# Performance work log

Hardware: AMD Instinct MI355X
Metric: run time of the kernel (lower is better)

Reference implementation:

```python
import jax, jax.numpy as jnp
import numpy as np

EPS = 1e-8

def _conv(x, w, b=None):
    # NCHW conv, stride 1, SAME padding (k=3, pad=1)
    y = jax.lax.conv_general_dilated(x, w, (1, 1), 'SAME',
                                     dimension_numbers=('NCHW', 'OIHW', 'NCHW'))
    if b is not None:
        y = y + b[None, :, None, None]
    return y

def setup_inputs() -> dict:
    key = jax.random.key(0)
    ks = jax.random.split(key, 6)
    B, C, H, W = 512, 1024, 8, 8
    return {
        'x': jax.random.normal(ks[0], (B, C, H, W), jnp.float32),
        'w1_1': jax.random.normal(ks[1], (1, 1, 3, 3), jnp.float32) * 0.1,
        'w5': jax.random.normal(ks[2], (4, 2, 3, 3), jnp.float32) * 0.1,
        'b5': jax.random.normal(ks[3], (4,), jnp.float32) * 0.1,
        'w6': jax.random.normal(ks[4], (1, 4, 3, 3), jnp.float32) * 0.1,
        'b6': jax.random.normal(ks[5], (1,), jnp.float32) * 0.1,
    }

def reference(x, w1_1, w5, b5, w6, b6):
    B, C, H, W = x.shape  # H == W == 8 by module construction
    m = jnp.max(x, axis=1, keepdims=True)  # [B,1,H,W] channel max
    # 2x2 non-overlapping windows, torch unfold layout -> [B,1,(H/2)*(W/2),4]
    win = m.reshape(B, 1, H // 2, 2, W // 2, 2)
    win = win.transpose(0, 1, 2, 4, 3, 5).reshape(B, 1, (H // 2) * (W // 2), 4)
    # probabilistic pooling: clean inf/nan/negatives, sample per window
    winc = jnp.where(jnp.isinf(win) | jnp.isnan(win) | (win < 0), EPS, win)
    skey = jax.random.key(1)
    idx = jax.random.categorical(skey, winc, axis=-1)  # softmax(winc) multinomial
    mo2 = jnp.take_along_axis(winc, idx[..., None], axis=-1)[..., 0]
    mo2 = mo2.reshape(B, 1, H // 2, W // 2)
    # adaptive max/avg pool (4,4) on 8x8 == 2x2 pooling, reuse windows
    mo3 = win.max(axis=-1).reshape(B, 1, H // 2, W // 2)
    ao4 = win.mean(axis=-1).reshape(B, 1, H // 2, W // 2)
    out2 = 0.1 * mo2 + 0.6 * mo3 + 0.3 * ao4
    out2 = _conv(out2, w1_1)  # bias-free 1->1 conv
    out2 = jax.image.resize(out2, (B, 1, H, W), method='bilinear')  # align_corners=False
    out1 = jnp.concatenate([m, out2], axis=1)  # [B,2,H,W]
    gate = jax.nn.sigmoid(_conv(jax.nn.relu(_conv(out1, w5, b5)), w6, b6))  # [B,1,H,W]
    return jax.nn.relu(x * gate)
```

## Files before the change

kernel.cpp:

```cpp
#include <hip/hip_runtime.h>
#include <math.h>

#define C_DIM 1024
#define HW 64
#define NT_A 512
#define NT_B 256
#define F4_PER_BATCH 16384
#define EPSV 1e-8f
#define TINYF 1.17549435e-38f

__device__ __forceinline__ void threefry2x32_01(unsigned x0, unsigned x1,
                                                unsigned& o0, unsigned& o1) {
    const unsigned ks0 = 0u, ks1 = 1u, ks2 = 0x1BD11BDBu;
    x0 += ks0; x1 += ks1;
#define TF_R(r) { x0 += x1; x1 = (x1 << (r)) | (x1 >> (32 - (r))); x1 ^= x0; }
    TF_R(13) TF_R(15) TF_R(26) TF_R(6)
    x0 += ks1; x1 += ks2 + 1u;
    TF_R(17) TF_R(29) TF_R(16) TF_R(24)
    x0 += ks2; x1 += ks0 + 2u;
    TF_R(13) TF_R(15) TF_R(26) TF_R(6)
    x0 += ks0; x1 += ks1 + 3u;
    TF_R(17) TF_R(29) TF_R(16) TF_R(24)
    x0 += ks1; x1 += ks2 + 4u;
    TF_R(13) TF_R(15) TF_R(26) TF_R(6)
    x0 += ks2; x1 += ks0 + 5u;
#undef TF_R
    o0 = x0; o1 = x1;
}

__device__ __forceinline__ unsigned jax_random_bits(unsigned n) {
    unsigned o0, o1;
    threefry2x32_01(0u, n, o0, o1);
    return o0 ^ o1;
}

__device__ __forceinline__ bool bad_val(float v) {
    return ((__float_as_uint(v) & 0x7F800000u) == 0x7F800000u) || (v < 0.0f);
}

__global__ __launch_bounds__(NT_A) void sa_gate_kernel(
    const float* __restrict__ x,
    const float* __restrict__ w11,
    const float* __restrict__ w5,
    const float* __restrict__ b5,
    const float* __restrict__ w6,
    const float* __restrict__ b6,
    float* __restrict__ gate_out)
{
    const int b = blockIdx.x;
    const int t = threadIdx.x;

    const float4* __restrict__ xb = (const float4*)x + (size_t)b * F4_PER_BATCH;

    __shared__ float4 red[8 * 16];
    __shared__ float sm[64];
    __shared__ float sa16[16];
    __shared__ float sb16[16];
    __shared__ float so2[64];
    __shared__ float shid[4 * 64];

    float4 pm = make_float4(-INFINITY, -INFINITY, -INFINITY, -INFINITY);
#pragma unroll 16
    for (int i = 0; i < 32; ++i) {
        float4 v = xb[t + NT_A * i];
        pm.x = fmaxf(pm.x, v.x); pm.y = fmaxf(pm.y, v.y);
        pm.z = fmaxf(pm.z, v.z); pm.w = fmaxf(pm.w, v.w);
    }
#pragma unroll
    for (int off = 16; off <= 32; off <<= 1) {
        pm.x = fmaxf(pm.x, __shfl_xor(pm.x, off, 64));
        pm.y = fmaxf(pm.y, __shfl_xor(pm.y, off, 64));
        pm.z = fmaxf(pm.z, __shfl_xor(pm.z, off, 64));
        pm.w = fmaxf(pm.w, __shfl_xor(pm.w, off, 64));
    }
    const int wv = t >> 6, lane = t & 63;
    if (lane < 16) red[wv * 16 + lane] = pm;
    __syncthreads();
    if (t >= 64) return;

    if (t < 16) {
        float4 a = red[t];
#pragma unroll
        for (int w = 1; w < 8; ++w) {
            float4 o = red[w * 16 + t];
            a.x = fmaxf(a.x, o.x); a.y = fmaxf(a.y, o.y);
            a.z = fmaxf(a.z, o.z); a.w = fmaxf(a.w, o.w);
        }
        sm[t * 4 + 0] = a.x; sm[t * 4 + 1] = a.y;
        sm[t * 4 + 2] = a.z; sm[t * 4 + 3] = a.w;
    }
    __builtin_amdgcn_wave_barrier();

    if (t < 16) {
        int h2 = t >> 2, w2 = t & 3;
        float win[4], winc[4], sg[4];
#pragma unroll
        for (int j = 0; j < 4; ++j) {
            int hh = 2 * h2 + (j >> 1), ww = 2 * w2 + (j & 1);
            float v = sm[hh * 8 + ww];
            win[j] = v;
            winc[j] = bad_val(v) ? EPSV : v;
            unsigned n = (unsigned)(b * 64 + t * 4 + j);
            unsigned bits = jax_random_bits(n);
            float f = __uint_as_float(0x3F800000u | (bits >> 9)) - 1.0f;
            float u = fmaxf(TINYF, f + TINYF);
            sg[j] = -logf(-logf(u));
        }
        int idx = 0;
        float best = winc[0] + sg[0];
#pragma unroll
        for (int j = 1; j < 4; ++j) {
            float s = winc[j] + sg[j];
            if (s > best) { best = s; idx = j; }
        }
        float mo2 = winc[idx];
        float mo3 = fmaxf(fmaxf(win[0], win[1]), fmaxf(win[2], win[3]));
        float ssum = ((win[0] + win[1]) + win[2]) + win[3];
        float ao4 = ssum * 0.25f;
        sa16[t] = 0.1f * mo2 + 0.6f * mo3 + 0.3f * ao4;
    }
    __builtin_amdgcn_wave_barrier();

    if (t < 16) {
        int i = t >> 2, j = t & 3;
        float acc = 0.0f;
#pragma unroll
        for (int dy = -1; dy <= 1; ++dy) {
            int yy = i + dy;
            if (yy < 0 || yy > 3) continue;
#pragma unroll
            for (int dx = -1; dx <= 1; ++dx) {
                int xx = j + dx;
                if (xx < 0 || xx > 3) continue;
                acc += sa16[yy * 4 + xx] * w11[(dy + 1) * 3 + (dx + 1)];
            }
        }
        sb16[t] = acc;
    }
    __builtin_amdgcn_wave_barrier();

    {
        int y = t >> 3, xx2 = t & 7;
        float sy = (y + 0.5f) * 0.5f - 0.5f;
        float sx = (xx2 + 0.5f) * 0.5f - 0.5f;
        float fy = fminf(fmaxf(sy, 0.0f), 3.0f);
        float fx = fminf(fmaxf(sx, 0.0f), 3.0f);
        int iy0 = (int)floorf(fy); int iy1 = min(iy0 + 1, 3); float ry = fy - (float)iy0;
        int ix0 = (int)floorf(fx); int ix1 = min(ix0 + 1, 3); float rx = fx - (float)ix0;
        float v00 = sb16[iy0 * 4 + ix0], v01 = sb16[iy0 * 4 + ix1];
        float v10 = sb16[iy1 * 4 + ix0], v11 = sb16[iy1 * 4 + ix1];
        float top = v00 * (1.0f - rx) + v01 * rx;
        float bot = v10 * (1.0f - rx) + v11 * rx;
        so2[t] = top * (1.0f - ry) + bot * ry;
    }
    __builtin_amdgcn_wave_barrier();

    {
        int y = t >> 3, x2 = t & 7;
        float a0 = b5[0], a1 = b5[1], a2 = b5[2], a3 = b5[3];
#pragma unroll
        for (int dy = -1; dy <= 1; ++dy) {
            int yy = y + dy;
            if (yy < 0 || yy > 7) continue;
#pragma unroll
            for (int dx = -1; dx <= 1; ++dx) {
                int xx = x2 + dx;
                if (xx < 0 || xx > 7) continue;
                float i0 = sm[yy * 8 + xx];
                float i1 = so2[yy * 8 + xx];
                int kk = (dy + 1) * 3 + (dx + 1);
                a0 += i0 * w5[0 * 18 + kk] + i1 * w5[0 * 18 + 9 + kk];
                a1 += i0 * w5[1 * 18 + kk] + i1 * w5[1 * 18 + 9 + kk];
                a2 += i0 * w5[2 * 18 + kk] + i1 * w5[2 * 18 + 9 + kk];
                a3 += i0 * w5[3 * 18 + kk] + i1 * w5[3 * 18 + 9 + kk];
            }
        }
        shid[0 * 64 + t] = fmaxf(a0, 0.0f);
        shid[1 * 64 + t] = fmaxf(a1, 0.0f);
        shid[2 * 64 + t] = fmaxf(a2, 0.0f);
        shid[3 * 64 + t] = fmaxf(a3, 0.0f);
    }
    __builtin_amdgcn_wave_barrier();

    {
        int y = t >> 3, x2 = t & 7;
        float acc = b6[0];
#pragma unroll
        for (int dy = -1; dy <= 1; ++dy) {
            int yy = y + dy;
            if (yy < 0 || yy > 7) continue;
#pragma unroll
            for (int dx = -1; dx <= 1; ++dx) {
                int xx = x2 + dx;
                if (xx < 0 || xx > 7) continue;
                int kk = (dy + 1) * 3 + (dx + 1);
                int p = yy * 8 + xx;
                acc += shid[0 * 64 + p] * w6[0 + kk]
                     + shid[1 * 64 + p] * w6[9 + kk]
                     + shid[2 * 64 + p] * w6[18 + kk]
                     + shid[3 * 64 + p] * w6[27 + kk];
            }
        }
        gate_out[b * 64 + t] = 1.0f / (1.0f + expf(-acc));
    }
}

__global__ __launch_bounds__(NT_B) void sa_apply_kernel(
    const float* __restrict__ x,
    const float* __restrict__ gate,
    float* __restrict__ out)
{
    const int bid = blockIdx.x;
    const int t = threadIdx.x;
    const int b = bid >> 2;
    const size_t base = (size_t)bid * 4096;

    const float4* __restrict__ x4 = (const float4*)x;
    float4* __restrict__ o4 = (float4*)out;

    const float4 gv = ((const float4*)(gate + b * 64))[t & 15];

#pragma unroll 8
    for (int i = 0; i < 16; ++i) {
        size_t idx = base + t + NT_B * i;
        float4 v = x4[idx];
        float4 o;
        o.x = fmaxf(v.x * gv.x, 0.0f);
        o.y = fmaxf(v.y * gv.y, 0.0f);
        o.z = fmaxf(v.z * gv.z, 0.0f);
        o.w = fmaxf(v.w * gv.w, 0.0f);
        o4[idx] = o;
    }
}

extern "C" void kernel_launch(void* const* d_in, const int* in_sizes, int n_in,
                              void* d_out, int out_size, void* d_ws, size_t ws_size,
                              hipStream_t stream) {
    const float* x   = (const float*)d_in[0];
    const float* w11 = (const float*)d_in[1];
    const float* w5  = (const float*)d_in[2];
    const float* b5  = (const float*)d_in[3];
    const float* w6  = (const float*)d_in[4];
    const float* b6  = (const float*)d_in[5];
    float* out  = (float*)d_out;
    float* gate = (float*)d_ws;

    int B = in_sizes[0] / (C_DIM * HW);
    sa_gate_kernel<<<dim3(B), dim3(NT_A), 0, stream>>>(x, w11, w5, b5, w6, b6, gate);
    sa_apply_kernel<<<dim3(B * 4), dim3(NT_B), 0, stream>>>(x, gate, out);
}
```

Baseline: 259.8 us.

## Split channel-max across blocks with atomics, separate tiny middle kernel, nontemporal stores

The channel-max reduction now runs over 4 blocks per batch instead of one 512-thread block. Partial maxima are combined with atomicMax on an order-preserving unsigned encoding of the floats, which gives more parallelism for the memory-bound read of x. The gate computation moves into its own 64-thread kernel. The apply kernel now uses twice as many blocks, each doing half the work, and writes with nontemporal stores. The trade-off is an extra memset and an extra kernel launch, plus atomic traffic.

Measured after the change: 266.4 us. +2.6%, slower.

```diff
diff --git a/kernel.cpp b/kernel.cpp
--- a/kernel.cpp
+++ b/kernel.cpp
@@ -3,11 +3,11 @@
 
 #define C_DIM 1024
 #define HW 64
-#define NT_A 512
-#define NT_B 256
 #define F4_PER_BATCH 16384
 #define EPSV 1e-8f
 #define TINYF 1.17549435e-38f
+
+typedef float vfloat4 __attribute__((ext_vector_type(4)));
 
 __device__ __forceinline__ void threefry2x32_01(unsigned x0, unsigned x1,
                                                 unsigned& o0, unsigned& o1) {
@@ -38,8 +38,59 @@
     return ((__float_as_uint(v) & 0x7F800000u) == 0x7F800000u) || (v < 0.0f);
 }
 
-__global__ __launch_bounds__(NT_A) void sa_gate_kernel(
-    const float* __restrict__ x,
+__device__ __forceinline__ unsigned enc_f32(float f) {
+    unsigned b = __float_as_uint(f);
+    return (b & 0x80000000u) ? ~b : (b | 0x80000000u);
+}
+__device__ __forceinline__ float dec_f32(unsigned u) {
+    unsigned b = (u & 0x80000000u) ? (u ^ 0x80000000u) : ~u;
+    return __uint_as_float(b);
+}
+
+__global__ __launch_bounds__(256) void sa_max_kernel(
+    const float* __restrict__ x, unsigned* __restrict__ maxenc)
+{
+    const int bid = blockIdx.x;
+    const int t = threadIdx.x;
+    const int b = bid >> 2;
+    const float4* __restrict__ xb = (const float4*)x + (size_t)bid * 4096;
+
+    float4 pm = make_float4(-INFINITY, -INFINITY, -INFINITY, -INFINITY);
+#pragma unroll 8
+    for (int i = 0; i < 16; ++i) {
+        float4 v = xb[t + 256 * i];
+        pm.x = fmaxf(pm.x, v.x); pm.y = fmaxf(pm.y, v.y);
+        pm.z = fmaxf(pm.z, v.z); pm.w = fmaxf(pm.w, v.w);
+    }
+#pragma unroll
+    for (int off = 16; off <= 32; off <<= 1) {
+        pm.x = fmaxf(pm.x, __shfl_xor(pm.x, off, 64));
+        pm.y = fmaxf(pm.y, __shfl_xor(pm.y, off, 64));
+        pm.z = fmaxf(pm.z, __shfl_xor(pm.z, off, 64));
+        pm.w = fmaxf(pm.w, __shfl_xor(pm.w, off, 64));
+    }
+    __shared__ float4 red[4][16];
+    const int wv = t >> 6, lane = t & 63;
+    if (lane < 16) red[wv][lane] = pm;
+    __syncthreads();
+    if (t < 16) {
+        float4 a = red[0][t];
+#pragma unroll
+        for (int w = 1; w < 4; ++w) {
+            float4 o = red[w][t];
+            a.x = fmaxf(a.x, o.x); a.y = fmaxf(a.y, o.y);
+            a.z = fmaxf(a.z, o.z); a.w = fmaxf(a.w, o.w);
+        }
+        unsigned* dst = maxenc + b * 64 + t * 4;
+        atomicMax(dst + 0, enc_f32(a.x));
+        atomicMax(dst + 1, enc_f32(a.y));
+        atomicMax(dst + 2, enc_f32(a.z));
+        atomicMax(dst + 3, enc_f32(a.w));
+    }
+}
+
+__global__ __launch_bounds__(64) void sa_middle_kernel(
+    const unsigned* __restrict__ maxenc,
     const float* __restrict__ w11,
     const float* __restrict__ w5,
     const float* __restrict__ b5,
@@ -50,46 +101,14 @@
     const int b = blockIdx.x;
     const int t = threadIdx.x;
 
-    const float4* __restrict__ xb = (const float4*)x + (size_t)b * F4_PER_BATCH;
-
-    __shared__ float4 red[8 * 16];
     __shared__ float sm[64];
     __shared__ float sa16[16];
     __shared__ float sb16[16];
     __shared__ float so2[64];
     __shared__ float shid[4 * 64];
 
-    float4 pm = make_float4(-INFINITY, -INFINITY, -INFINITY, -INFINITY);
-#pragma unroll 16
-    for (int i = 0; i < 32; ++i) {
-        float4 v = xb[t + NT_A * i];
-        pm.x = fmaxf(pm.x, v.x); pm.y = fmaxf(pm.y, v.y);
-        pm.z = fmaxf(pm.z, v.z); pm.w = fmaxf(pm.w, v.w);
-    }
-#pragma unroll
-    for (int off = 16; off <= 32; off <<= 1) {
-        pm.x = fmaxf(pm.x, __shfl_xor(pm.x, off, 64));
-        pm.y = fmaxf(pm.y, __shfl_xor(pm.y, off, 64));
-        pm.z = fmaxf(pm.z, __shfl_xor(pm.z, off, 64));
-        pm.w = fmaxf(pm.w, __shfl_xor(pm.w, off, 64));
-    }
-    const int wv = t >> 6, lane = t & 63;
-    if (lane < 16) red[wv * 16 + lane] = pm;
-    __syncthreads();
-    if (t >= 64) return;
-
-    if (t < 16) {
-        float4 a = red[t];
-#pragma unroll
-        for (int w = 1; w < 8; ++w) {
-            float4 o = red[w * 16 + t];
-            a.x = fmaxf(a.x, o.x); a.y = fmaxf(a.y, o.y);
-            a.z = fmaxf(a.z, o.z); a.w = fmaxf(a.w, o.w);
-        }
-        sm[t * 4 + 0] = a.x; sm[t * 4 + 1] = a.y;
-        sm[t * 4 + 2] = a.z; sm[t * 4 + 3] = a.w;
-    }
-    __builtin_amdgcn_wave_barrier();
+    sm[t] = dec_f32(maxenc[b * 64 + t]);
+    __syncthreads();
 
     if (t < 16) {
         int h2 = t >> 2, w2 = t & 3;
@@ -119,7 +138,7 @@
         float ao4 = ssum * 0.25f;
         sa16[t] = 0.1f * mo2 + 0.6f * mo3 + 0.3f * ao4;
     }
-    __builtin_amdgcn_wave_barrier();
+    __syncthreads();
 
     if (t < 16) {
         int i = t >> 2, j = t & 3;
@@ -137,7 +156,7 @@
         }
         sb16[t] = acc;
     }
-    __builtin_amdgcn_wave_barrier();
+    __syncthreads();
 
     {
         int y = t >> 3, xx2 = t & 7;
@@ -153,7 +172,7 @@
         float bot = v10 * (1.0f - rx) + v11 * rx;
         so2[t] = top * (1.0f - ry) + bot * ry;
     }
-    __builtin_amdgcn_wave_barrier();
+    __syncthreads();
 
     {
         int y = t >> 3, x2 = t & 7;
@@ -180,7 +199,7 @@
         shid[2 * 64 + t] = fmaxf(a2, 0.0f);
         shid[3 * 64 + t] = fmaxf(a3, 0.0f);
     }
-    __builtin_amdgcn_wave_barrier();
+    __syncthreads();
 
     {
         int y = t >> 3, x2 = t & 7;
@@ -205,31 +224,31 @@
     }
 }
 
-__global__ __launch_bounds__(NT_B) void sa_apply_kernel(
+__global__ __launch_bounds__(256) void sa_apply_kernel(
     const float* __restrict__ x,
     const float* __restrict__ gate,
     float* __restrict__ out)
 {
     const int bid = blockIdx.x;
     const int t = threadIdx.x;
-    const int b = bid >> 2;
-    const size_t base = (size_t)bid * 4096;
-
-    const float4* __restrict__ x4 = (const float4*)x;
-    float4* __restrict__ o4 = (float4*)out;
+    const int b = bid >> 3;
+    const size_t base = (size_t)bid * 2048;
+
+    const vfloat4* __restrict__ x4 = (const vfloat4*)x;
+    vfloat4* __restrict__ o4 = (vfloat4*)out;
 
     const float4 gv = ((const float4*)(gate + b * 64))[t & 15];
 
-#pragma unroll 8
-    for (int i = 0; i < 16; ++i) {
-        size_t idx = base + t + NT_B * i;
-        float4 v = x4[idx];
-        float4 o;
+#pragma unroll
+    for (int i = 0; i < 8; ++i) {
+        size_t idx = base + t + 256 * i;
+        vfloat4 v = x4[idx];
+        vfloat4 o;
         o.x = fmaxf(v.x * gv.x, 0.0f);
         o.y = fmaxf(v.y * gv.y, 0.0f);
         o.z = fmaxf(v.z * gv.z, 0.0f);
         o.w = fmaxf(v.w * gv.w, 0.0f);
-        o4[idx] = o;
+        __builtin_nontemporal_store(o, &o4[idx]);
     }
 }
 
@@ -242,10 +261,14 @@
     const float* b5  = (const float*)d_in[3];
     const float* w6  = (const float*)d_in[4];
     const float* b6  = (const float*)d_in[5];
-    float* out  = (float*)d_out;
-    float* gate = (float*)d_ws;
+    float* out = (float*)d_out;
 
     int B = in_sizes[0] / (C_DIM * HW);
-    sa_gate_kernel<<<dim3(B), dim3(NT_A), 0, stream>>>(x, w11, w5, b5, w6, b6, gate);
-    sa_apply_kernel<<<dim3(B * 4), dim3(NT_B), 0, stream>>>(x, gate, out);
-}
+    unsigned* maxenc = (unsigned*)d_ws;
+    float* gate = (float*)d_ws + (size_t)B * 64;
+
+    (void)hipMemsetAsync(maxenc, 0, (size_t)B * 64 * sizeof(unsigned), stream);
+    sa_max_kernel<<<dim3(B * 4), dim3(256), 0, stream>>>(x, maxenc);
+    sa_middle_kernel<<<dim3(B), dim3(64), 0, stream>>>(maxenc, w11, w5, b5, w6, b6, gate);
+    sa_apply_kernel<<<dim3(B * 8), dim3(256), 0, stream>>>(x, gate, out);
+}
```
